# Performance work log

Measured on AMD Instinct MI355X. Metric: run time of the kernel, lower is better.

The kernel has to match this reference:

```python
import jax, jax.numpy as jnp
import numpy as np

TAU = 0.5
N, D = 8192, 128


def _l2norm(x):
    return x / jnp.linalg.norm(x, axis=-1, keepdims=True)


def setup_inputs() -> dict:
    key = jax.random.key(0)
    k1, k2 = jax.random.split(key)
    # Projected + L2-normalized node embeddings (output of GRACE._encode)
    z1 = _l2norm(jax.random.normal(k1, (N, D), dtype=jnp.float32))
    z2 = _l2norm(jax.random.normal(k2, (N, D), dtype=jnp.float32))
    return {"z1": z1, "z2": z2}


def reference(z1, z2):
    # refl_sim = exp(z1 z1^T / tau), between_sim = exp(z1 z2^T / tau)
    refl = jnp.exp(jnp.matmul(z1, z1.T) / TAU)        # [N, N]
    between = jnp.exp(jnp.matmul(z1, z2.T) / TAU)     # [N, N]

    def half_loss(a, b):
        # positives = diag(b); negatives = off-diag of a and b per row.
        # denom = (rowsum(a) - diag(a)) + (rowsum(b) - diag(b)) + diag(b)
        pos = jnp.diagonal(b)
        denom = a.sum(axis=1) - jnp.diagonal(a) + b.sum(axis=1)
        return -jnp.log(pos / denom)

    l1 = half_loss(refl, between)      # row view
    l2 = half_loss(refl.T, between.T)  # column view (diag is shared)
    ret = 0.5 * (l1 + l2)
    return ret.mean()
```

## Files before the change

### kernel.cpp

```cpp
#include <hip/hip_runtime.h>

typedef __attribute__((ext_vector_type(8))) short bf16x8;
typedef __attribute__((ext_vector_type(4))) float f32x4;
typedef unsigned short u16;
typedef unsigned int u32;

constexpr int N = 8192;
constexpr int D = 128;
constexpr float CEXP   = 2.8853900817779268f;
constexpr float BSCALE = 1.6986435688113073f;

#if __has_builtin(__builtin_amdgcn_exp2f)
__device__ __forceinline__ float fexp2(float x) { return __builtin_amdgcn_exp2f(x); }
#else
__device__ __forceinline__ float fexp2(float x) { return exp2f(x); }
#endif

__device__ __forceinline__ u32 f2bf(float x) {
  union { float f; unsigned u; } v;
  v.f = x;
  unsigned r = v.u + 0x7fffu + ((v.u >> 16) & 1u);
  return r >> 16;
}

__global__ void convert_dots_kernel(const float2* __restrict__ z1, const float2* __restrict__ z2,
                                    u32* __restrict__ o1, u32* __restrict__ o2,
                                    float* __restrict__ dotSelf, float* __restrict__ dotCross,
                                    float* __restrict__ zeroBase, float* __restrict__ out) {
  const int tid = threadIdx.x;
  const int row = blockIdx.x * 4 + (tid >> 6);
  const int l = tid & 63;
  const int zidx = blockIdx.x * 256 + tid;
  if (zidx < 3 * N) zeroBase[zidx] = 0.0f;
  if (zidx == 0) out[0] = 0.0f;

  float2 a = z1[row * 64 + l];
  float2 b = z2[row * 64 + l];
  o1[row * 64 + l] = f2bf(a.x * BSCALE) | (f2bf(a.y * BSCALE) << 16);
  o2[row * 64 + l] = f2bf(b.x * BSCALE) | (f2bf(b.y * BSCALE) << 16);

  float d11 = a.x * a.x + a.y * a.y;
  float d12 = a.x * b.x + a.y * b.y;
#pragma unroll
  for (int mask = 1; mask < 64; mask <<= 1) {
    d11 += __shfl_xor(d11, mask);
    d12 += __shfl_xor(d12, mask);
  }
  if (l == 0) {
    dotSelf[row] = d11;
    dotCross[row] = d12;
  }
}

__device__ __forceinline__ void stage16k(char* lds, const char* gsrc, int soff, int doff) {
#pragma unroll
  for (int s = 0; s < 4; ++s) {
    __builtin_amdgcn_global_load_lds(
        (const __attribute__((address_space(1))) u32*)(gsrc + soff + s * 4096),
        (__attribute__((address_space(3))) u32*)(lds + doff + s * 4096), 16, 0, 0);
  }
}

__global__ __launch_bounds__(256, 4) void gemm_kernel(const u16* __restrict__ z1b,
                                                      const u16* __restrict__ z2b,
                                                      float* __restrict__ rowRefl,
                                                      float* __restrict__ rowBet,
                                                      float* __restrict__ colBet) {
  __shared__ __align__(16) char B0[16384];
  __shared__ __align__(16) char B1[16384];
  const int tid = threadIdx.x;
  const int l = tid & 63, w = tid >> 6;
  const int lr = l & 15, lg = l >> 4;
  const int bi = blockIdx.x >> 4;
  const int jg = blockIdx.x & 15;
  const bool between = jg >= 8;
  const u16* bsrc = between ? z2b : z1b;
  const int colbase = (jg & 7) * 1024;

  const int soff = (tid >> 4) * 256 + (((tid & 15) ^ (tid >> 4)) << 4);
  const int doff = tid * 16;

  stage16k(B0, (const char*)(z1b + (size_t)bi * 64 * D), soff, doff);
  __syncthreads();
  bf16x8 af[4][4];
#pragma unroll
  for (int m = 0; m < 4; ++m)
#pragma unroll
    for (int kk = 0; kk < 4; ++kk)
      af[m][kk] = *(const bf16x8*)(B0 + (m * 16 + lr) * 256 + (((kk * 4 + lg) ^ lr) << 4));
  __syncthreads();

  stage16k(B0, (const char*)(bsrc + (size_t)colbase * D), soff, doff);

  float rowp[4][4];
#pragma unroll
  for (int m = 0; m < 4; ++m)
#pragma unroll
    for (int r = 0; r < 4; ++r) rowp[m][r] = 0.f;

  for (int t = 0; t < 16; ++t) {
    __syncthreads();
    const char* cur = (t & 1) ? B1 : B0;
    char* nxt = (t & 1) ? B0 : B1;
    if (t + 1 < 16)
      stage16k(nxt, (const char*)(bsrc + (size_t)(colbase + (t + 1) * 64) * D), soff, doff);

    bf16x8 bfr[4];
#pragma unroll
    for (int kk = 0; kk < 4; ++kk)
      bfr[kk] = *(const bf16x8*)(cur + (w * 16 + lr) * 256 + (((kk * 4 + lg) ^ lr) << 4));

    f32x4 acc[4];
    const f32x4 z4 = {0.f, 0.f, 0.f, 0.f};
#pragma unroll
    for (int m = 0; m < 4; ++m)
      acc[m] = __builtin_amdgcn_mfma_f32_16x16x32_bf16(af[m][0], bfr[0], z4, 0, 0, 0);
#pragma unroll
    for (int kk = 1; kk < 4; ++kk)
#pragma unroll
      for (int m = 0; m < 4; ++m)
        acc[m] = __builtin_amdgcn_mfma_f32_16x16x32_bf16(af[m][kk], bfr[kk], acc[m], 0, 0, 0);

    if (!between) {
#pragma unroll
      for (int m = 0; m < 4; ++m)
#pragma unroll
        for (int r = 0; r < 4; ++r) rowp[m][r] += fexp2(acc[m][r]);
    } else {
      float colp = 0.f;
#pragma unroll
      for (int m = 0; m < 4; ++m) {
        float v0 = fexp2(acc[m][0]), v1 = fexp2(acc[m][1]);
        float v2 = fexp2(acc[m][2]), v3 = fexp2(acc[m][3]);
        rowp[m][0] += v0;
        rowp[m][1] += v1;
        rowp[m][2] += v2;
        rowp[m][3] += v3;
        colp += (v0 + v1) + (v2 + v3);
      }
      colp += __shfl_xor(colp, 16);
      colp += __shfl_xor(colp, 32);
      if (l < 16) atomicAdd(&colBet[colbase + t * 64 + w * 16 + l], colp);
    }
  }

  float* rowdst = between ? rowBet : rowRefl;
#pragma unroll
  for (int m = 0; m < 4; ++m)
#pragma unroll
    for (int r = 0; r < 4; ++r) {
      float s = rowp[m][r];
      s += __shfl_xor(s, 1);
      s += __shfl_xor(s, 2);
      s += __shfl_xor(s, 4);
      s += __shfl_xor(s, 8);
      if (lr == 0) atomicAdd(&rowdst[bi * 64 + m * 16 + lg * 4 + r], s);
    }
}

__global__ void final_kernel(const float* __restrict__ rowRefl, const float* __restrict__ rowBet,
                             const float* __restrict__ colBet, const float* __restrict__ dotSelf,
                             const float* __restrict__ dotCross, float* __restrict__ out) {
  const int r = blockIdx.x * 256 + threadIdx.x;
  float rdiag = fexp2(dotSelf[r] * CEXP);
  float base = rowRefl[r] - rdiag;
  float loss = 0.5f * (logf(base + rowBet[r]) + logf(base + colBet[r])) - 2.0f * dotCross[r];
  loss *= (1.0f / (float)N);
#pragma unroll
  for (int mask = 1; mask < 64; mask <<= 1) loss += __shfl_xor(loss, mask);
  if ((threadIdx.x & 63) == 0) atomicAdd(out, loss);
}

extern "C" void kernel_launch(void* const* d_in, const int* in_sizes, int n_in,
                              void* d_out, int out_size, void* d_ws, size_t ws_size,
                              hipStream_t stream) {
  const float* z1 = (const float*)d_in[0];
  const float* z2 = (const float*)d_in[1];
  float* out = (float*)d_out;
  char* ws = (char*)d_ws;

  u16* z1b = (u16*)ws;
  u16* z2b = (u16*)(ws + (size_t)N * D * 2);
  float* rowRefl = (float*)(ws + (size_t)2 * N * D * 2);
  float* rowBet = rowRefl + N;
  float* colBet = rowBet + N;
  float* dotSelf = colBet + N;
  float* dotCross = dotSelf + N;

  convert_dots_kernel<<<N / 4, 256, 0, stream>>>((const float2*)z1, (const float2*)z2,
                                                 (u32*)z1b, (u32*)z2b, dotSelf, dotCross,
                                                 rowRefl, out);
  gemm_kernel<<<2048, 256, 0, stream>>>(z1b, z2b, rowRefl, rowBet, colBet);
  final_kernel<<<N / 256, 256, 0, stream>>>(rowRefl, rowBet, colBet, dotSelf, dotCross, out);
}
```

Before: 65.24 us.

## Give each wave its own B staging buffers and drop block barriers in main loop

Each wave now stages only its own 16-row slice of the B panel into a private double-buffered LDS region, using per-wave vmcnt waits instead of block-wide __syncthreads in the 16-step loop. Column-sum atomics are buffered in LDS and flushed after the loop, so global atomics no longer sit inside it. Launch bounds drop from 4 to 3 blocks per CU. The aim is to remove barrier stalls and let waves run independently, at the cost of lower occupancy and reliance on hand-placed waitcnt correctness for the async LDS loads.

```diff
diff --git a/kernel.cpp b/kernel.cpp
--- a/kernel.cpp
+++ b/kernel.cpp
@@ -52,22 +52,24 @@
   }
 }
 
-__device__ __forceinline__ void stage16k(char* lds, const char* gsrc, int soff, int doff) {
+__device__ __forceinline__ void stageB(char* ldsbase, const char* gpanel, int l) {
 #pragma unroll
   for (int s = 0; s < 4; ++s) {
+    const int r = s * 4 + (l >> 4);
+    const int src = r * 256 + (((l & 15) ^ r) << 4);
     __builtin_amdgcn_global_load_lds(
-        (const __attribute__((address_space(1))) u32*)(gsrc + soff + s * 4096),
-        (__attribute__((address_space(3))) u32*)(lds + doff + s * 4096), 16, 0, 0);
-  }
-}
-
-__global__ __launch_bounds__(256, 4) void gemm_kernel(const u16* __restrict__ z1b,
+        (const __attribute__((address_space(1))) u32*)(gpanel + src),
+        (__attribute__((address_space(3))) u32*)(ldsbase + s * 1024 + l * 16), 16, 0, 0);
+  }
+}
+
+__global__ __launch_bounds__(256, 3) void gemm_kernel(const u16* __restrict__ z1b,
                                                       const u16* __restrict__ z2b,
                                                       float* __restrict__ rowRefl,
                                                       float* __restrict__ rowBet,
                                                       float* __restrict__ colBet) {
-  __shared__ __align__(16) char B0[16384];
-  __shared__ __align__(16) char B1[16384];
+  __shared__ __align__(16) char Bbuf[32768];
+  __shared__ float colLds[4][256];
   const int tid = threadIdx.x;
   const int l = tid & 63, w = tid >> 6;
   const int lr = l & 15, lg = l >> 4;
@@ -77,20 +79,28 @@
   const u16* bsrc = between ? z2b : z1b;
   const int colbase = (jg & 7) * 1024;
 
-  const int soff = (tid >> 4) * 256 + (((tid & 15) ^ (tid >> 4)) << 4);
-  const int doff = tid * 16;
-
-  stage16k(B0, (const char*)(z1b + (size_t)bi * 64 * D), soff, doff);
+  {
+    const int soff = (tid >> 4) * 256 + (((tid & 15) ^ (tid >> 4)) << 4);
+    const char* gA = (const char*)(z1b + (size_t)bi * 64 * D);
+#pragma unroll
+    for (int s = 0; s < 4; ++s) {
+      __builtin_amdgcn_global_load_lds(
+          (const __attribute__((address_space(1))) u32*)(gA + soff + s * 4096),
+          (__attribute__((address_space(3))) u32*)(Bbuf + tid * 16 + s * 4096), 16, 0, 0);
+    }
+  }
   __syncthreads();
   bf16x8 af[4][4];
 #pragma unroll
   for (int m = 0; m < 4; ++m)
 #pragma unroll
     for (int kk = 0; kk < 4; ++kk)
-      af[m][kk] = *(const bf16x8*)(B0 + (m * 16 + lr) * 256 + (((kk * 4 + lg) ^ lr) << 4));
+      af[m][kk] = *(const bf16x8*)(Bbuf + (m * 16 + lr) * 256 + (((kk * 4 + lg) ^ lr) << 4));
   __syncthreads();
-
-  stage16k(B0, (const char*)(bsrc + (size_t)colbase * D), soff, doff);
+  asm volatile("" ::: "memory");
+
+  char* myBuf = Bbuf + w * 8192;
+  const char* gB = (const char*)bsrc + (size_t)(colbase + w * 16) * 256;
 
   float rowp[4][4];
 #pragma unroll
@@ -98,17 +108,21 @@
 #pragma unroll
     for (int r = 0; r < 4; ++r) rowp[m][r] = 0.f;
 
+  stageB(myBuf, gB, l);
+
   for (int t = 0; t < 16; ++t) {
-    __syncthreads();
-    const char* cur = (t & 1) ? B1 : B0;
-    char* nxt = (t & 1) ? B0 : B1;
-    if (t + 1 < 16)
-      stage16k(nxt, (const char*)(bsrc + (size_t)(colbase + (t + 1) * 64) * D), soff, doff);
+    const char* cur = myBuf + (t & 1) * 4096;
+    if (t < 15) {
+      stageB(myBuf + ((t + 1) & 1) * 4096, gB + (size_t)(t + 1) * 16384, l);
+      asm volatile("s_waitcnt vmcnt(4)" ::: "memory");
+    } else {
+      asm volatile("s_waitcnt vmcnt(0)" ::: "memory");
+    }
 
     bf16x8 bfr[4];
 #pragma unroll
     for (int kk = 0; kk < 4; ++kk)
-      bfr[kk] = *(const bf16x8*)(cur + (w * 16 + lr) * 256 + (((kk * 4 + lg) ^ lr) << 4));
+      bfr[kk] = *(const bf16x8*)(cur + lr * 256 + (((kk * 4 + lg) ^ lr) << 4));
 
     f32x4 acc[4];
     const f32x4 z4 = {0.f, 0.f, 0.f, 0.f};
@@ -140,8 +154,14 @@
       }
       colp += __shfl_xor(colp, 16);
       colp += __shfl_xor(colp, 32);
-      if (l < 16) atomicAdd(&colBet[colbase + t * 64 + w * 16 + l], colp);
-    }
+      if (l < 16) colLds[w][t * 16 + l] = colp;
+    }
+  }
+
+  if (between && l < 16) {
+#pragma unroll
+    for (int t = 0; t < 16; ++t)
+      atomicAdd(&colBet[colbase + t * 64 + w * 16 + l], colLds[w][t * 16 + l]);
   }
 
   float* rowdst = between ? rowBet : rowRefl;
```

New measurement: 71.72 us. +9.9%, slower.
